# Kernel optimization log

Measured on AMD Instinct MI355X. Metric: run time of the kernel, lower is better.

The kernel has to match this reference:

```python
import jax, jax.numpy as jnp
import numpy as np

N = 8192
FEAT = 200
SEG = FEAT // 4  # 50
OUT = 300


def setup_inputs() -> dict:
    key = jax.random.key(0)
    ks = jax.random.split(key, 10)
    x = jax.random.normal(ks[0], (N, FEAT), dtype=jnp.float32)
    # row-normalized-ish dense adjacencies so activations stay O(1)
    A_S = jax.random.uniform(ks[1], (N, N), dtype=jnp.float32) / N
    A_F = jax.random.uniform(ks[2], (N, N), dtype=jnp.float32) / N
    gcn_W = jax.random.normal(ks[3], (SEG, SEG), dtype=jnp.float32) / np.sqrt(SEG)
    gcn_b = jnp.zeros((SEG,), dtype=jnp.float32)
    # 12 forget gates: order s1,s2,s3,f1,f2,f3,s1b,s2b,s3b,f1b,f2b,f3b
    gates_W = jax.random.normal(ks[4], (12, 2 * SEG, SEG), dtype=jnp.float32)
    gates_b = jax.random.normal(ks[5], (12, SEG), dtype=jnp.float32)
    proj_W = jax.random.normal(ks[6], (8 * SEG, OUT), dtype=jnp.float32) / np.sqrt(8 * SEG)
    proj_b = jnp.zeros((OUT,), dtype=jnp.float32)
    return {"x": x, "A_S": A_S, "A_F": A_F, "gcn_W": gcn_W, "gcn_b": gcn_b,
            "gates_W": gates_W, "gates_b": gates_b, "proj_W": proj_W, "proj_b": proj_b}


def _lgfm(x, A_S, A_F, gcn_W, gcn_b, gates_W, gates_b, proj_W, proj_b):
    seg = x.shape[1] // 4

    def gcn(h, A):
        # Kipf GraphConvolution: relu(A @ (h @ W) + b); dropout inactive (eval)
        return jax.nn.relu(A @ (h @ gcn_W) + gcn_b)

    def gate(i, h1, h2):
        a = jax.nn.sigmoid(jnp.concatenate([h1, h2], axis=1) @ gates_W[i] + gates_b[i])
        return a * h1

    GS1, GS2, GS3, GF1, GF2, GF3 = 0, 1, 2, 3, 4, 5
    GS1B, GS2B, GS3B, GF1B, GF2B, GF3B = 6, 7, 8, 9, 10, 11

    x1, x2, x3, x4 = x[:, :seg], x[:, seg:2 * seg], x[:, 2 * seg:3 * seg], x[:, 3 * seg:]

    # forward branch (F path then S gating)
    t1_XF1 = x1 + gcn(x1, A_F)
    t1_XS1 = gcn(x1, A_S)
    t1_XF2 = 0.2 * t1_XS1 + 0.8 * gcn(t1_XF1, A_F)
    t2_XF1 = x2 + gcn(x2, A_F)
    t2_XS1 = gcn(x2, A_S)
    t2_XS1 = t2_XS1 + gate(GS1, t1_XS1, t2_XS1)
    t2_XF2 = 0.2 * t2_XS1 + 0.8 * gcn(t2_XF1, A_F)
    t2_XF2 = gate(GF1, t1_XF2, t2_XF2) + t2_XF2
    t3_XF1 = 0.2 * x3 + 0.8 * gcn(x3, A_F)
    t3_XS1 = gcn(x3, A_S)
    t3_XS1 = t3_XS1 + gate(GS2, t2_XS1, t3_XS1)
    t3_XF2 = 0.2 * t3_XS1 + 0.8 * gcn(t3_XF1, A_F)
    t3_XF2 = gate(GF2, t2_XF2, t3_XF2) + t3_XF2
    t4_XF1 = x4 + gcn(x4, A_F)
    t4_XS1 = gcn(x4, A_S)
    t4_XS1 = t4_XS1 + gate(GS3, t3_XS1, t4_XS1)
    t4_XF2 = 0.2 * t4_XS1 + 0.8 * gcn(t4_XF1, A_F)
    t4_XF2 = gate(GF3, t3_XF2, t4_XF2) + t4_XF2

    # mirrored branch (S path then F gating)
    t1_XS1b = x1 + gcn(x1, A_S)
    t1_XF1b = gcn(x1, A_F)
    t1_XS2 = 0.2 * t1_XF1b + 0.8 * gcn(t1_XS1b, A_S)
    t2_XS1b = x2 + gcn(x2, A_S)
    t2_XF1b = gcn(x2, A_F)
    t2_XF1b = t2_XF1b + gate(GF1B, t1_XF1b, t2_XF1b)
    t2_XS2 = 0.2 * t2_XF1b + 0.8 * gcn(t2_XS1b, A_S)
    t2_XS2 = gate(GS1B, t1_XS2, t2_XS2) + t2_XS2
    t3_XS1b = 0.2 * x3 + 0.8 * gcn(x3, A_S)
    t3_XF1b = gcn(x3, A_F)
    t3_XF1b = t3_XF1b + gate(GF2B, t2_XF1b, t3_XF1b)
    t3_XS2 = 0.2 * t3_XF1b + 0.8 * gcn(t3_XS1b, A_S)
    t3_XS2 = gate(GS2B, t2_XS2, t3_XS2) + t3_XS2
    t4_XS1b = x4 + gcn(x4, A_S)
    t4_XF1b = gcn(x4, A_F)
    t4_XF1b = t4_XF1b + gate(GF3B, t3_XF1b, t4_XF1b)
    t4_XS2 = 0.2 * t4_XF1b + 0.8 * gcn(t4_XS1b, A_S)
    t4_XS2 = gate(GS3B, t3_XS2, t4_XS2) + t4_XS2

    h_L = jnp.concatenate([t1_XF2, t1_XS2, t2_XF2, t2_XS2,
                           t3_XF2, t3_XS2, t4_XF2, t4_XS2], axis=1)
    return h_L @ proj_W + proj_b


def reference(x, A_S, A_F, gcn_W, gcn_b, gates_W, gates_b, proj_W, proj_b):
    return _lgfm(x, A_S, A_F, gcn_W, gcn_b, gates_W, gates_b, proj_W, proj_b)
```

## Files before the change

### kernel.cpp

```cpp
#include <hip/hip_runtime.h>
#include <math.h>

typedef float float4v __attribute__((ext_vector_type(4)));
typedef __attribute__((ext_vector_type(4))) float f32x4;
typedef __attribute__((ext_vector_type(8))) short short8v;
typedef __attribute__((ext_vector_type(8))) unsigned short ushort8v;

#define NROW 8192
#define FEAT 200
#define OUTC 300
#define ZLD  256
#define HLK  448
#define HLN  384

__device__ __forceinline__ unsigned short f2bf(float x) {
  unsigned u = __float_as_uint(x);
  return (unsigned short)((u + 0x7fffu + ((u >> 16) & 1u)) >> 16);
}

__global__ __launch_bounds__(256) void conv2_bf16_kernel(
    const float* __restrict__ AF, const float* __restrict__ AS,
    unsigned short* __restrict__ AbF, unsigned short* __restrict__ AbS) {
  int blk = blockIdx.x;
  const float* A = (blk < 8192) ? AF : AS;
  unsigned short* Ab = (blk < 8192) ? AbF : AbS;
  size_t tid = (size_t)(blk & 8191) * 256 + threadIdx.x;
  const float4v* A4 = (const float4v*)A;
  ushort8v* O8 = (ushort8v*)Ab;
  for (size_t b = tid * 2; b < 16777216ull; b += (size_t)8192 * 256 * 2) {
    float4v v0 = __builtin_nontemporal_load(&A4[b]);
    float4v v1 = __builtin_nontemporal_load(&A4[b + 1]);
    ushort8v o;
    o[0] = f2bf(v0[0]); o[1] = f2bf(v0[1]); o[2] = f2bf(v0[2]); o[3] = f2bf(v0[3]);
    o[4] = f2bf(v1[0]); o[5] = f2bf(v1[1]); o[6] = f2bf(v1[2]); o[7] = f2bf(v1[3]);
    __builtin_nontemporal_store(o, &O8[b >> 1]);
  }
}

__global__ __launch_bounds__(256) void zmul_t_kernel(
    const float* __restrict__ x, const float* __restrict__ W,
    unsigned short* __restrict__ Zt) {
  __shared__ float Ws[2500];
  __shared__ float hs[16][200];
  __shared__ float zbuf[16][256];
  int t = threadIdx.x;
  int r0 = blockIdx.x * 16;
  for (int i = t; i < 2500; i += 256) Ws[i] = W[i];
  for (int i = t; i < 16 * FEAT; i += 256)
    hs[0][i] = x[(size_t)r0 * FEAT + i];
  __syncthreads();
  for (int i = t; i < 16 * 256; i += 256) {
    int row = i >> 8, j = i & 255;
    float acc = 0.f;
    if (j < FEAT) {
      int s = j / 50, jj = j % 50;
      const float* hrow = &hs[row][s * 50];
      #pragma unroll 5
      for (int k = 0; k < 50; ++k) acc += hrow[k] * Ws[k * 50 + jj];
    }
    zbuf[row][j] = acc;
  }
  __syncthreads();
  unsigned int* Ztu = (unsigned int*)Zt;
  for (int i = t; i < 256 * 8; i += 256) {
    int j = i >> 3, w2 = i & 7;
    unsigned int lo = f2bf(zbuf[2 * w2][j]);
    unsigned int hi = f2bf(zbuf[2 * w2 + 1][j]);
    Ztu[((j * NROW + r0) >> 1) + w2] = lo | (hi << 16);
  }
}

__global__ __launch_bounds__(256, 2) void gemm_pair_kernel(
    const unsigned short* __restrict__ AbF,
    const unsigned short* __restrict__ AbS,
    const unsigned short* __restrict__ ZtF,
    const unsigned short* __restrict__ ZtS,
    float* __restrict__ Cpart) {
  int d = blockIdx.x;
  int L = (d & 7) * 64 + (d >> 3);
  int mat = L & 1;
  int ks  = (L >> 1) & 1;
  int cb  = (L >> 2) & 1;
  int rb  = L >> 3;

  const unsigned short* __restrict__ Ab = mat ? AbS : AbF;
  const unsigned short* __restrict__ Zt = mat ? ZtS : ZtF;

  int t = threadIdx.x;
  int lane = t & 63, wv = t >> 6;
  int row0 = rb * 128, n0 = cb * 128, k0 = ks * 4096;

  __shared__ short As[2][128 * 64];
  __shared__ short Bs[2][128 * 64];

  int srcA[4], srcB[4], ldsDst[4];
  #pragma unroll
  for (int i = 0; i < 4; ++i) {
    int c = i * 256 + t;
    int m = c >> 3, sl = c & 7;
    int sw = ((sl ^ (m & 7)) * 8);
    srcA[i] = (row0 + m) * NROW + sw;
    srcB[i] = (n0 + m) * NROW + sw;
    ldsDst[i] = (i * 256 + wv * 64) * 8;
  }

#define STAGE_TILE(buf, kt)                                                          \
  {                                                                                  \
    _Pragma("unroll")                                                                \
    for (int i = 0; i < 4; ++i) {                                                    \
      __builtin_amdgcn_global_load_lds(                                              \
          (const __attribute__((address_space(1))) void*)(Ab + srcA[i] + (kt)),      \
          (__attribute__((address_space(3))) void*)(&As[buf][ldsDst[i]]), 16, 0, 0); \
      __builtin_amdgcn_global_load_lds(                                              \
          (const __attribute__((address_space(1))) void*)(Zt + srcB[i] + (kt)),      \
          (__attribute__((address_space(3))) void*)(&Bs[buf][ldsDst[i]]), 16, 0, 0); \
    }                                                                                \
  }

  f32x4 acc[4][4];
  #pragma unroll
  for (int i = 0; i < 4; ++i)
    #pragma unroll
    for (int j = 0; j < 4; ++j) acc[i][j] = (f32x4)0.f;

  int m0 = (wv >> 1) * 64, n0w = (wv & 1) * 64;
  int l15 = lane & 15, l4 = lane >> 4;

  int cur = 0;
  STAGE_TILE(0, k0)
  __syncthreads();

  for (int it = 0; it < 64; ++it) {
    if (it + 1 < 64) STAGE_TILE(cur ^ 1, k0 + (it + 1) * 64)

    #pragma unroll
    for (int kk = 0; kk < 2; ++kk) {
      int slot = kk * 4 + l4;
      short8v a[4], b[4];
      #pragma unroll
      for (int i = 0; i < 4; ++i) {
        int m = m0 + i * 16 + l15;
        a[i] = *(const short8v*)&As[cur][m * 64 + ((slot ^ (m & 7)) * 8)];
        int n = n0w + i * 16 + l15;
        b[i] = *(const short8v*)&Bs[cur][n * 64 + ((slot ^ (n & 7)) * 8)];
      }
      #pragma unroll
      for (int i = 0; i < 4; ++i)
        #pragma unroll
        for (int j = 0; j < 4; ++j)
          acc[i][j] = __builtin_amdgcn_mfma_f32_16x16x32_bf16(a[i], b[j], acc[i][j], 0, 0, 0);
    }
    __syncthreads();
    cur ^= 1;
  }
#undef STAGE_TILE

  int s = mat * 2 + ks;
  #pragma unroll
  for (int i = 0; i < 4; ++i) {
    #pragma unroll
    for (int j = 0; j < 4; ++j) {
      int c = n0 + n0w + j * 16 + l15;
      #pragma unroll
      for (int q = 0; q < 4; ++q) {
        int r = row0 + m0 + i * 16 + l4 * 4 + q;
        Cpart[((size_t)(s * NROW + r) << 8) + c] = acc[i][j][q];
      }
    }
  }
}

__global__ __launch_bounds__(256) void reduce_zmul_kernel(
    const float* __restrict__ Cpart, const float* __restrict__ bias,
    const float* __restrict__ x, const float* __restrict__ W,
    float* __restrict__ GF0, float* __restrict__ GS0,
    unsigned short* __restrict__ ZtF, unsigned short* __restrict__ ZtS) {
  __shared__ float Ws[2500];
  __shared__ float hs[16][200];
  __shared__ float zbuf[16][256];
  int t = threadIdx.x;
  int r0 = blockIdx.x * 16;
  int w = t >> 6, j = t & 63;
  bool act = j < 50;
  int rbase = r0 + w * 4;
  for (int i = t; i < 2500; i += 256) Ws[i] = W[i];

  const float alpha[4] = {1.f, 1.f, 0.2f, 1.f};
  const float beta[4]  = {1.f, 1.f, 0.8f, 1.f};
  float gf[4][4], gs[4][4];
  if (act) {
    float bv = bias[j];
    #pragma unroll
    for (int r = 0; r < 4; ++r)
      #pragma unroll
      for (int s = 0; s < 4; ++s) {
        int c = s * 50 + j;
        size_t base = (((size_t)(rbase + r)) << 8) + c;
        float vF = Cpart[base] + Cpart[base + (size_t)NROW * 256];
        float vS = Cpart[base + (size_t)2 * NROW * 256] + Cpart[base + (size_t)3 * NROW * 256];
        gf[r][s] = fmaxf(vF + bv, 0.f);
        gs[r][s] = fmaxf(vS + bv, 0.f);
        GF0[(size_t)(rbase + r) * FEAT + c] = gf[r][s];
        GS0[(size_t)(rbase + r) * FEAT + c] = gs[r][s];
      }
    #pragma unroll
    for (int r = 0; r < 4; ++r)
      #pragma unroll
      for (int s = 0; s < 4; ++s)
        hs[w * 4 + r][s * 50 + j] =
            alpha[s] * x[(size_t)(rbase + r) * FEAT + s * 50 + j] + beta[s] * gf[r][s];
  }
  __syncthreads();
  for (int i = t; i < 16 * 256; i += 256) {
    int row = i >> 8, jj = i & 255;
    float acc = 0.f;
    if (jj < FEAT) {
      int s = jj / 50, j2 = jj % 50;
      const float* hrow = &hs[row][s * 50];
      #pragma unroll 5
      for (int k = 0; k < 50; ++k) acc += hrow[k] * Ws[k * 50 + j2];
    }
    zbuf[row][jj] = acc;
  }
  __syncthreads();
  {
    unsigned int* Ztu = (unsigned int*)ZtF;
    for (int i = t; i < 256 * 8; i += 256) {
      int j2 = i >> 3, w2 = i & 7;
      unsigned int lo = f2bf(zbuf[2 * w2][j2]);
      unsigned int hi = f2bf(zbuf[2 * w2 + 1][j2]);
      Ztu[((j2 * NROW + r0) >> 1) + w2] = lo | (hi << 16);
    }
  }
  if (act) {
    #pragma unroll
    for (int r = 0; r < 4; ++r)
      #pragma unroll
      for (int s = 0; s < 4; ++s)
        hs[w * 4 + r][s * 50 + j] =
            alpha[s] * x[(size_t)(rbase + r) * FEAT + s * 50 + j] + beta[s] * gs[r][s];
  }
  __syncthreads();
  for (int i = t; i < 16 * 256; i += 256) {
    int row = i >> 8, jj = i & 255;
    float acc = 0.f;
    if (jj < FEAT) {
      int s = jj / 50, j2 = jj % 50;
      const float* hrow = &hs[row][s * 50];
      #pragma unroll 5
      for (int k = 0; k < 50; ++k) acc += hrow[k] * Ws[k * 50 + j2];
    }
    zbuf[row][jj] = acc;
  }
  __syncthreads();
  {
    unsigned int* Ztu = (unsigned int*)ZtS;
    for (int i = t; i < 256 * 8; i += 256) {
      int j2 = i >> 3, w2 = i & 7;
      unsigned int lo = f2bf(zbuf[2 * w2][j2]);
      unsigned int hi = f2bf(zbuf[2 * w2 + 1][j2]);
      Ztu[((j2 * NROW + r0) >> 1) + w2] = lo | (hi << 16);
    }
  }
}

__device__ __forceinline__ void gate4(const float* __restrict__ gWi, const float* __restrict__ gbi,
                                      float* hsw, float* Wg, int t, int j, bool act,
                                      const float* h1, const float* h2, float* aout) {
  if (act) {
    #pragma unroll
    for (int r = 0; r < 4; ++r) { hsw[r * 128 + j] = h1[r]; hsw[r * 128 + 64 + j] = h2[r]; }
  }
  {
    const float4v* src = (const float4v*)gWi;
    float4v* dst = (float4v*)Wg;
    #pragma unroll
    for (int u = 0; u < 5; ++u) {
      int i = t + 256 * u;
      if (i < 1250) dst[i] = src[i];
    }
  }
  __syncthreads();
  float acc0 = 0.f, acc1 = 0.f, acc2 = 0.f, acc3 = 0.f;
  if (act) {
    float bv = gbi[j];
    acc0 = bv; acc1 = bv; acc2 = bv; acc3 = bv;
    #pragma unroll 2
    for (int k = 0; k < 50; ++k) {
      float wv = Wg[k * 50 + j];
      acc0 += hsw[0 * 128 + k] * wv;
      acc1 += hsw[1 * 128 + k] * wv;
      acc2 += hsw[2 * 128 + k] * wv;
      acc3 += hsw[3 * 128 + k] * wv;
    }
    #pragma unroll 2
    for (int k = 0; k < 50; ++k) {
      float wv = Wg[(50 + k) * 50 + j];
      acc0 += hsw[0 * 128 + 64 + k] * wv;
      acc1 += hsw[1 * 128 + 64 + k] * wv;
      acc2 += hsw[2 * 128 + 64 + k] * wv;
      acc3 += hsw[3 * 128 + 64 + k] * wv;
    }
  }
  __syncthreads();
  float accs[4] = {acc0, acc1, acc2, acc3};
  #pragma unroll
  for (int r = 0; r < 4; ++r) {
    float a = 1.f / (1.f + expf(-accs[r]));
    aout[r] = a * h1[r];
  }
}

__global__ __launch_bounds__(256) void reduce_chain_kernel(
    const float* __restrict__ Cpart, const float* __restrict__ bias,
    const float* __restrict__ GF0, const float* __restrict__ GS0,
    const float* __restrict__ gW, const float* __restrict__ gb,
    unsigned short* __restrict__ hLb) {
  __shared__ float hsb[4 * 512];
  __shared__ float Wg[5000];
  int t = threadIdx.x;
  int w = t >> 6, j = t & 63;
  bool act = j < 50;
  float* hsw = &hsb[w * 512];
  int rbase = blockIdx.x * 16 + w * 4;

  float gf0[4][4], gs0[4][4], gf1[4][4], gs1[4][4];
  if (act) {
    float bv = bias[j];
    #pragma unroll
    for (int r = 0; r < 4; ++r)
      #pragma unroll
      for (int s = 0; s < 4; ++s) {
        int c = s * 50 + j;
        size_t base = (((size_t)(rbase + r)) << 8) + c;
        float vF = Cpart[base] + Cpart[base + (size_t)NROW * 256];
        float vS = Cpart[base + (size_t)2 * NROW * 256] + Cpart[base + (size_t)3 * NROW * 256];
        gf1[r][s] = fmaxf(vF + bv, 0.f);
        gs1[r][s] = fmaxf(vS + bv, 0.f);
        gf0[r][s] = GF0[(size_t)(rbase + r) * FEAT + c];
        gs0[r][s] = GS0[(size_t)(rbase + r) * FEAT + c];
      }
  }
  if (!act) {
    for (int p = j - 50; p < 48; p += 14)
      #pragma unroll
      for (int r = 0; r < 4; ++r)
        hLb[(size_t)(rbase + r) * HLK + 400 + p] = 0;
  }

  float xf2[4], xs1[4], pre[4], a[4], h1t[4], h2t[4];
  #pragma unroll
  for (int r = 0; r < 4; ++r) xf2[r] = 0.2f * gs0[r][0] + 0.8f * gf1[r][0];
  if (act) {
    #pragma unroll
    for (int r = 0; r < 4; ++r) hLb[(size_t)(rbase + r) * HLK + 0 + j] = f2bf(xf2[r]);
  }
  #pragma unroll
  for (int r = 0; r < 4; ++r) { h1t[r] = gs0[r][0]; h2t[r] = gs0[r][1]; }
  gate4(gW + 0 * 5000, gb + 0 * 50, hsw, Wg, t, j, act, h1t, h2t, a);
  #pragma unroll
  for (int r = 0; r < 4; ++r) xs1[r] = gs0[r][1] + a[r];
  #pragma unroll
  for (int r = 0; r < 4; ++r) pre[r] = 0.2f * xs1[r] + 0.8f * gf1[r][1];
  gate4(gW + 3 * 5000, gb + 3 * 50, hsw, Wg, t, j, act, xf2, pre, a);
  #pragma unroll
  for (int r = 0; r < 4; ++r) xf2[r] = a[r] + pre[r];
  if (act) {
    #pragma unroll
    for (int r = 0; r < 4; ++r) hLb[(size_t)(rbase + r) * HLK + 100 + j] = f2bf(xf2[r]);
  }
  #pragma unroll
  for (int r = 0; r < 4; ++r) { h1t[r] = xs1[r]; h2t[r] = gs0[r][2]; }
  gate4(gW + 1 * 5000, gb + 1 * 50, hsw, Wg, t, j, act, h1t, h2t, a);
  #pragma unroll
  for (int r = 0; r < 4; ++r) xs1[r] = gs0[r][2] + a[r];
  #pragma unroll
  for (int r = 0; r < 4; ++r) pre[r] = 0.2f * xs1[r] + 0.8f * gf1[r][2];
  gate4(gW + 4 * 5000, gb + 4 * 50, hsw, Wg, t, j, act, xf2, pre, a);
  #pragma unroll
  for (int r = 0; r < 4; ++r) xf2[r] = a[r] + pre[r];
  if (act) {
    #pragma unroll
    for (int r = 0; r < 4; ++r) hLb[(size_t)(rbase + r) * HLK + 200 + j] = f2bf(xf2[r]);
  }
  #pragma unroll
  for (int r = 0; r < 4; ++r) { h1t[r] = xs1[r]; h2t[r] = gs0[r][3]; }
  gate4(gW + 2 * 5000, gb + 2 * 50, hsw, Wg, t, j, act, h1t, h2t, a);
  #pragma unroll
  for (int r = 0; r < 4; ++r) xs1[r] = gs0[r][3] + a[r];
  #pragma unroll
  for (int r = 0; r < 4; ++r) pre[r] = 0.2f * xs1[r] + 0.8f * gf1[r][3];
  gate4(gW + 5 * 5000, gb + 5 * 50, hsw, Wg, t, j, act, xf2, pre, a);
  #pragma unroll
  for (int r = 0; r < 4; ++r) xf2[r] = a[r] + pre[r];
  if (act) {
    #pragma unroll
    for (int r = 0; r < 4; ++r) hLb[(size_t)(rbase + r) * HLK + 300 + j] = f2bf(xf2[r]);
  }

  float xs2[4], xf1b[4];
  #pragma unroll
  for (int r = 0; r < 4; ++r) xs2[r] = 0.2f * gf0[r][0] + 0.8f * gs1[r][0];
  if (act) {
    #pragma unroll
    for (int r = 0; r < 4; ++r) hLb[(size_t)(rbase + r) * HLK + 50 + j] = f2bf(xs2[r]);
  }
  #pragma unroll
  for (int r = 0; r < 4; ++r) { h1t[r] = gf0[r][0]; h2t[r] = gf0[r][1]; }
  gate4(gW + 9 * 5000, gb + 9 * 50, hsw, Wg, t, j, act, h1t, h2t, a);
  #pragma unroll
  for (int r = 0; r < 4; ++r) xf1b[r] = gf0[r][1] + a[r];
  #pragma unroll
  for (int r = 0; r < 4; ++r) pre[r] = 0.2f * xf1b[r] + 0.8f * gs1[r][1];
  gate4(gW + 6 * 5000, gb + 6 * 50, hsw, Wg, t, j, act, xs2, pre, a);
  #pragma unroll
  for (int r = 0; r < 4; ++r) xs2[r] = a[r] + pre[r];
  if (act) {
    #pragma unroll
    for (int r = 0; r < 4; ++r) hLb[(size_t)(rbase + r) * HLK + 150 + j] = f2bf(xs2[r]);
  }
  #pragma unroll
  for (int r = 0; r < 4; ++r) { h1t[r] = xf1b[r]; h2t[r] = gf0[r][2]; }
  gate4(gW + 10 * 5000, gb + 10 * 50, hsw, Wg, t, j, act, h1t, h2t, a);
  #pragma unroll
  for (int r = 0; r < 4; ++r) xf1b[r] = gf0[r][2] + a[r];
  #pragma unroll
  for (int r = 0; r < 4; ++r) pre[r] = 0.2f * xf1b[r] + 0.8f * gs1[r][2];
  gate4(gW + 7 * 5000, gb + 7 * 50, hsw, Wg, t, j, act, xs2, pre, a);
  #pragma unroll
  for (int r = 0; r < 4; ++r) xs2[r] = a[r] + pre[r];
  if (act) {
    #pragma unroll
    for (int r = 0; r < 4; ++r) hLb[(size_t)(rbase + r) * HLK + 250 + j] = f2bf(xs2[r]);
  }
  #pragma unroll
  for (int r = 0; r < 4; ++r) { h1t[r] = xf1b[r]; h2t[r] = gf0[r][3]; }
  gate4(gW + 11 * 5000, gb + 11 * 50, hsw, Wg, t, j, act, h1t, h2t, a);
  #pragma unroll
  for (int r = 0; r < 4; ++r) xf1b[r] = gf0[r][3] + a[r];
  #pragma unroll
  for (int r = 0; r < 4; ++r) pre[r] = 0.2f * xf1b[r] + 0.8f * gs1[r][3];
  gate4(gW + 8 * 5000, gb + 8 * 50, hsw, Wg, t, j, act, xs2, pre, a);
  #pragma unroll
  for (int r = 0; r < 4; ++r) xs2[r] = a[r] + pre[r];
  if (act) {
    #pragma unroll
    for (int r = 0; r < 4; ++r) hLb[(size_t)(rbase + r) * HLK + 350 + j] = f2bf(xs2[r]);
  }
}

__global__ __launch_bounds__(256) void wconv_kernel(
    const float* __restrict__ pW, unsigned short* __restrict__ Wtb) {
  int i = blockIdx.x * 256 + threadIdx.x;
  if (i >= HLN * HLK) return;
  int n = i / HLK, k = i % HLK;
  float v = (n < OUTC && k < 400) ? pW[k * OUTC + n] : 0.f;
  Wtb[i] = f2bf(v);
}

__global__ __launch_bounds__(256, 2) void proj_gemm_kernel(
    const unsigned short* __restrict__ hLb,
    const unsigned short* __restrict__ Wtb,
    const float* __restrict__ pb, float* __restrict__ outp) {
  int d = blockIdx.x;
  int L = (d & 7) * 24 + (d >> 3);
  int rb = L / 3, cb = L % 3;

  int t = threadIdx.x;
  int lane = t & 63, wv = t >> 6;
  int row0 = rb * 128, n0 = cb * 128;

  __shared__ short As[2][128 * 64];
  __shared__ short Bs[2][128 * 64];

  int srcA[4], srcB[4], ldsDst[4];
  #pragma unroll
  for (int i = 0; i < 4; ++i) {
    int c = i * 256 + t;
    int m = c >> 3, sl = c & 7;
    int sw = ((sl ^ (m & 7)) * 8);
    srcA[i] = (row0 + m) * HLK + sw;
    srcB[i] = (n0 + m) * HLK + sw;
    ldsDst[i] = (i * 256 + wv * 64) * 8;
  }

#define STAGE_TILE(buf, kt)                                                          \
  {                                                                                  \
    _Pragma("unroll")                                                                \
    for (int i = 0; i < 4; ++i) {                                                    \
      __builtin_amdgcn_global_load_lds(                                              \
          (const __attribute__((address_space(1))) void*)(hLb + srcA[i] + (kt)),     \
          (__attribute__((address_space(3))) void*)(&As[buf][ldsDst[i]]), 16, 0, 0); \
      __builtin_amdgcn_global_load_lds(                                              \
          (const __attribute__((address_space(1))) void*)(Wtb + srcB[i] + (kt)),     \
          (__attribute__((address_space(3))) void*)(&Bs[buf][ldsDst[i]]), 16, 0, 0); \
    }                                                                                \
  }

  f32x4 acc[4][4];
  #pragma unroll
  for (int i = 0; i < 4; ++i)
    #pragma unroll
    for (int j = 0; j < 4; ++j) acc[i][j] = (f32x4)0.f;

  int m0 = (wv >> 1) * 64, n0w = (wv & 1) * 64;
  int l15 = lane & 15, l4 = lane >> 4;

  int cur = 0;
  STAGE_TILE(0, 0)
  __syncthreads();

  for (int it = 0; it < 7; ++it) {
    if (it + 1 < 7) STAGE_TILE(cur ^ 1, (it + 1) * 64)

    #pragma unroll
    for (int kk = 0; kk < 2; ++kk) {
      int slot = kk * 4 + l4;
      short8v a[4], b[4];
      #pragma unroll
      for (int i = 0; i < 4; ++i) {
        int m = m0 + i * 16 + l15;
        a[i] = *(const short8v*)&As[cur][m * 64 + ((slot ^ (m & 7)) * 8)];
        int n = n0w + i * 16 + l15;
        b[i] = *(const short8v*)&Bs[cur][n * 64 + ((slot ^ (n & 7)) * 8)];
      }
      #pragma unroll
      for (int i = 0; i < 4; ++i)
        #pragma unroll
        for (int j = 0; j < 4; ++j)
          acc[i][j] = __builtin_amdgcn_mfma_f32_16x16x32_bf16(a[i], b[j], acc[i][j], 0, 0, 0);
    }
    __syncthreads();
    cur ^= 1;
  }
#undef STAGE_TILE

  #pragma unroll
  for (int i = 0; i < 4; ++i) {
    #pragma unroll
    for (int j = 0; j < 4; ++j) {
      int c = n0 + n0w + j * 16 + l15;
      if (c < OUTC) {
        float b = pb[c];
        #pragma unroll
        for (int q = 0; q < 4; ++q) {
          int r = row0 + m0 + i * 16 + l4 * 4 + q;
          outp[(size_t)r * OUTC + c] = acc[i][j][q] + b;
        }
      }
    }
  }
}

__global__ __launch_bounds__(256) void zmul_f32_kernel(
    const float* __restrict__ x, const float* __restrict__ g,
    const float* __restrict__ W,
    float a0, float a1, float a2, float a3,
    float b0, float b1, float b2, float b3,
    float* __restrict__ Zp) {
  __shared__ float Ws[2500];
  __shared__ float hs[200];
  int t = threadIdx.x;
  for (int i = t; i < 2500; i += 256) Ws[i] = W[i];
  float alpha[4] = {a0, a1, a2, a3};
  float beta[4]  = {b0, b1, b2, b3};
  int s  = (t < 200) ? (t / 50) : 0;
  int jj = (t < 200) ? (t % 50) : 0;
  int r0 = blockIdx.x * 32;
  for (int rr = 0; rr < 32; ++rr) {
    int row = r0 + rr;
    __syncthreads();
    if (t < 200) hs[t] = alpha[s] * x[row * FEAT + t] + beta[s] * g[row * FEAT + t];
    __syncthreads();
    float acc = 0.f;
    if (t < 200) {
      const float* hrow = &hs[s * 50];
      #pragma unroll 5
      for (int k = 0; k < 50; ++k) acc += hrow[k] * Ws[k * 50 + jj];
    }
    Zp[row * ZLD + t] = (t < 200) ? acc : 0.f;
  }
}

#define BM 64
#define BN 64
#define BK 32
#define ALD 68
__global__ __launch_bounds__(256) void gemm_relu_kernel(
    const float* __restrict__ A, const float* __restrict__ Zp,
    const float* __restrict__ bias, float* __restrict__ C) {
  int wg  = blockIdx.x;
  int swz = (wg & 7) * 64 + (wg >> 3);
  int rb  = swz >> 2;
  int cb  = swz & 3;
  int t   = threadIdx.x;
  int rt  = t >> 4, ct = t & 15;
  __shared__ __align__(16) float As[BK][ALD];
  __shared__ __align__(16) float Zs[BK][BN];
  float acc[4][4];
  #pragma unroll
  for (int i = 0; i < 4; ++i)
    #pragma unroll
    for (int j = 0; j < 4; ++j) acc[i][j] = 0.f;
  const int row0 = rb * BM, col0 = cb * BN;
  int ar = t >> 3;
  int ak = (t & 7) * 4;
  int zr = t >> 4;
  int zc = (t & 15) * 4;
  const float4v* A4 = (const float4v*)A;
  const float4v* Z4 = (const float4v*)Zp;
  float4v a0, a1, z0, z1;
  a0 = A4[((size_t)(row0 + ar) * NROW + 0 + ak) >> 2];
  a1 = A4[((size_t)(row0 + ar + 32) * NROW + 0 + ak) >> 2];
  z0 = Z4[((0 + zr) * ZLD + col0 + zc) >> 2];
  z1 = Z4[((0 + zr + 16) * ZLD + col0 + zc) >> 2];
  for (int kt = 0; kt < NROW; kt += BK) {
    __syncthreads();
    #pragma unroll
    for (int u = 0; u < 4; ++u) As[ak + u][ar] = a0[u];
    #pragma unroll
    for (int u = 0; u < 4; ++u) As[ak + u][ar + 32] = a1[u];
    *(float4v*)&Zs[zr][zc]      = z0;
    *(float4v*)&Zs[zr + 16][zc] = z1;
    __syncthreads();
    int kn = kt + BK;
    if (kn < NROW) {
      a0 = A4[((size_t)(row0 + ar) * NROW + kn + ak) >> 2];
      a1 = A4[((size_t)(row0 + ar + 32) * NROW + kn + ak) >> 2];
      z0 = Z4[((kn + zr) * ZLD + col0 + zc) >> 2];
      z1 = Z4[((kn + zr + 16) * ZLD + col0 + zc) >> 2];
    }
    #pragma unroll
    for (int k = 0; k < BK; ++k) {
      float4v av = *(const float4v*)&As[k][rt * 4];
      float4v zv = *(const float4v*)&Zs[k][ct * 4];
      #pragma unroll
      for (int i = 0; i < 4; ++i)
        #pragma unroll
        for (int j = 0; j < 4; ++j) acc[i][j] += av[i] * zv[j];
    }
  }
  #pragma unroll
  for (int i = 0; i < 4; ++i) {
    int grow = row0 + rt * 4 + i;
    #pragma unroll
    for (int j = 0; j < 4; ++j) {
      int gcol = col0 + ct * 4 + j;
      if (gcol < FEAT) {
        float v = acc[i][j] + bias[gcol % 50];
        C[(size_t)grow * FEAT + gcol] = fmaxf(v, 0.f);
      }
    }
  }
}

__global__ __launch_bounds__(256) void chain_top_kernel(
    const float* __restrict__ GS0, const float* __restrict__ GF1,
    const float* __restrict__ gW, const float* __restrict__ gb,
    unsigned short* __restrict__ hLb) {
  __shared__ float hsb[4 * 512];
  __shared__ float Wg[5000];
  int t = threadIdx.x;
  int w = t >> 6, j = t & 63;
  bool act = j < 50;
  float* hsw = &hsb[w * 512];
  int rbase = blockIdx.x * 16 + w * 4;
  float gs[4][4], gf[4][4];
  #pragma unroll
  for (int r = 0; r < 4; ++r)
    #pragma unroll
    for (int s = 0; s < 4; ++s) { gs[r][s] = 0.f; gf[r][s] = 0.f; }
  if (act) {
    #pragma unroll
    for (int r = 0; r < 4; ++r)
      #pragma unroll
      for (int s = 0; s < 4; ++s) {
        gs[r][s] = GS0[(size_t)(rbase + r) * FEAT + s * 50 + j];
        gf[r][s] = GF1[(size_t)(rbase + r) * FEAT + s * 50 + j];
      }
  }
  float xf2[4], xs1[4], pre[4], a[4], h1t[4], h2t[4];
  #pragma unroll
  for (int r = 0; r < 4; ++r) xf2[r] = 0.2f * gs[r][0] + 0.8f * gf[r][0];
  if (act) {
    #pragma unroll
    for (int r = 0; r < 4; ++r) hLb[(size_t)(rbase + r) * HLK + 0 + j] = f2bf(xf2[r]);
  }
  #pragma unroll
  for (int r = 0; r < 4; ++r) { h1t[r] = gs[r][0]; h2t[r] = gs[r][1]; }
  gate4(gW + 0 * 5000, gb + 0 * 50, hsw, Wg, t, j, act, h1t, h2t, a);
  #pragma unroll
  for (int r = 0; r < 4; ++r) xs1[r] = gs[r][1] + a[r];
  #pragma unroll
  for (int r = 0; r < 4; ++r) pre[r] = 0.2f * xs1[r] + 0.8f * gf[r][1];
  gate4(gW + 3 * 5000, gb + 3 * 50, hsw, Wg, t, j, act, xf2, pre, a);
  #pragma unroll
  for (int r = 0; r < 4; ++r) xf2[r] = a[r] + pre[r];
  if (act) {
    #pragma unroll
    for (int r = 0; r < 4; ++r) hLb[(size_t)(rbase + r) * HLK + 100 + j] = f2bf(xf2[r]);
  }
  #pragma unroll
  for (int r = 0; r < 4; ++r) { h1t[r] = xs1[r]; h2t[r] = gs[r][2]; }
  gate4(gW + 1 * 5000, gb + 1 * 50, hsw, Wg, t, j, act, h1t, h2t, a);
  #pragma unroll
  for (int r = 0; r < 4; ++r) xs1[r] = gs[r][2] + a[r];
  #pragma unroll
  for (int r = 0; r < 4; ++r) pre[r] = 0.2f * xs1[r] + 0.8f * gf[r][2];
  gate4(gW + 4 * 5000, gb + 4 * 50, hsw, Wg, t, j, act, xf2, pre, a);
  #pragma unroll
  for (int r = 0; r < 4; ++r) xf2[r] = a[r] + pre[r];
  if (act) {
    #pragma unroll
    for (int r = 0; r < 4; ++r) hLb[(size_t)(rbase + r) * HLK + 200 + j] = f2bf(xf2[r]);
  }
  #pragma unroll
  for (int r = 0; r < 4; ++r) { h1t[r] = xs1[r]; h2t[r] = gs[r][3]; }
  gate4(gW + 2 * 5000, gb + 2 * 50, hsw, Wg, t, j, act, h1t, h2t, a);
  #pragma unroll
  for (int r = 0; r < 4; ++r) xs1[r] = gs[r][3] + a[r];
  #pragma unroll
  for (int r = 0; r < 4; ++r) pre[r] = 0.2f * xs1[r] + 0.8f * gf[r][3];
  gate4(gW + 5 * 5000, gb + 5 * 50, hsw, Wg, t, j, act, xf2, pre, a);
  #pragma unroll
  for (int r = 0; r < 4; ++r) xf2[r] = a[r] + pre[r];
  if (act) {
    #pragma unroll
    for (int r = 0; r < 4; ++r) hLb[(size_t)(rbase + r) * HLK + 300 + j] = f2bf(xf2[r]);
  }
}

__global__ __launch_bounds__(256) void chain_bottom_kernel(
    const float* __restrict__ GF0, const float* __restrict__ GS1,
    const float* __restrict__ gW, const float* __restrict__ gb,
    unsigned short* __restrict__ hLb) {
  __shared__ float hsb[4 * 512];
  __shared__ float Wg[5000];
  int t = threadIdx.x;
  int w = t >> 6, j = t & 63;
  bool act = j < 50;
  float* hsw = &hsb[w * 512];
  int rbase = blockIdx.x * 16 + w * 4;
  float gf0[4][4], gs1[4][4];
  #pragma unroll
  for (int r = 0; r < 4; ++r)
    #pragma unroll
    for (int s = 0; s < 4; ++s) { gf0[r][s] = 0.f; gs1[r][s] = 0.f; }
  if (act) {
    #pragma unroll
    for (int r = 0; r < 4; ++r)
      #pragma unroll
      for (int s = 0; s < 4; ++s) {
        gf0[r][s] = GF0[(size_t)(rbase + r) * FEAT + s * 50 + j];
        gs1[r][s] = GS1[(size_t)(rbase + r) * FEAT + s * 50 + j];
      }
  }
  float xs2[4], xf1b[4], pre[4], a[4], h1t[4], h2t[4];
  #pragma unroll
  for (int r = 0; r < 4; ++r) xs2[r] = 0.2f * gf0[r][0] + 0.8f * gs1[r][0];
  if (act) {
    #pragma unroll
    for (int r = 0; r < 4; ++r) hLb[(size_t)(rbase + r) * HLK + 50 + j] = f2bf(xs2[r]);
  }
  #pragma unroll
  for (int r = 0; r < 4; ++r) { h1t[r] = gf0[r][0]; h2t[r] = gf0[r][1]; }
  gate4(gW + 9 * 5000, gb + 9 * 50, hsw, Wg, t, j, act, h1t, h2t, a);
  #pragma unroll
  for (int r = 0; r < 4; ++r) xf1b[r] = gf0[r][1] + a[r];
  #pragma unroll
  for (int r = 0; r < 4; ++r) pre[r] = 0.2f * xf1b[r] + 0.8f * gs1[r][1];
  gate4(gW + 6 * 5000, gb + 6 * 50, hsw, Wg, t, j, act, xs2, pre, a);
  #pragma unroll
  for (int r = 0; r < 4; ++r) xs2[r] = a[r] + pre[r];
  if (act) {
    #pragma unroll
    for (int r = 0; r < 4; ++r) hLb[(size_t)(rbase + r) * HLK + 150 + j] = f2bf(xs2[r]);
  }
  #pragma unroll
  for (int r = 0; r < 4; ++r) { h1t[r] = xf1b[r]; h2t[r] = gf0[r][2]; }
  gate4(gW + 10 * 5000, gb + 10 * 50, hsw, Wg, t, j, act, h1t, h2t, a);
  #pragma unroll
  for (int r = 0; r < 4; ++r) xf1b[r] = gf0[r][2] + a[r];
  #pragma unroll
  for (int r = 0; r < 4; ++r) pre[r] = 0.2f * xf1b[r] + 0.8f * gs1[r][2];
  gate4(gW + 7 * 5000, gb + 7 * 50, hsw, Wg, t, j, act, xs2, pre, a);
  #pragma unroll
  for (int r = 0; r < 4; ++r) xs2[r] = a[r] + pre[r];
  if (act) {
    #pragma unroll
    for (int r = 0; r < 4; ++r) hLb[(size_t)(rbase + r) * HLK + 250 + j] = f2bf(xs2[r]);
  }
  #pragma unroll
  for (int r = 0; r < 4; ++r) { h1t[r] = xf1b[r]; h2t[r] = gf0[r][3]; }
  gate4(gW + 11 * 5000, gb + 11 * 50, hsw, Wg, t, j, act, h1t, h2t, a);
  #pragma unroll
  for (int r = 0; r < 4; ++r) xf1b[r] = gf0[r][3] + a[r];
  #pragma unroll
  for (int r = 0; r < 4; ++r) pre[r] = 0.2f * xf1b[r] + 0.8f * gs1[r][3];
  gate4(gW + 8 * 5000, gb + 8 * 50, hsw, Wg, t, j, act, xs2, pre, a);
  #pragma unroll
  for (int r = 0; r < 4; ++r) xs2[r] = a[r] + pre[r];
  if (act) {
    #pragma unroll
    for (int r = 0; r < 4; ++r) hLb[(size_t)(rbase + r) * HLK + 350 + j] = f2bf(xs2[r]);
  }
}

extern "C" void kernel_launch(void* const* d_in, const int* in_sizes, int n_in,
                              void* d_out, int out_size, void* d_ws, size_t ws_size,
                              hipStream_t stream) {
  const float* x       = (const float*)d_in[0];
  const float* A_S     = (const float*)d_in[1];
  const float* A_F     = (const float*)d_in[2];
  const float* gcn_W   = (const float*)d_in[3];
  const float* gcn_b   = (const float*)d_in[4];
  const float* gates_W = (const float*)d_in[5];
  const float* gates_b = (const float*)d_in[6];
  const float* proj_W  = (const float*)d_in[7];
  const float* proj_b  = (const float*)d_in[8];
  float* out = (float*)d_out;

  const size_t szAb    = (size_t)NROW * NROW * 2;
  const size_t szZt    = (size_t)256 * NROW * 2;
  const size_t szCpart = (size_t)4 * NROW * 256 * 4;
  const size_t szG     = (size_t)NROW * FEAT * 4;
  const size_t szHLb   = (size_t)NROW * HLK * 2;
  const size_t szWtb   = (size_t)HLN * HLK * 2;
  const size_t need = 2 * szAb + 3 * szZt + szCpart + 2 * szG + szHLb + szWtb;

  if (ws_size >= need) {
    char* w = (char*)d_ws;
    unsigned short* AbF  = (unsigned short*)w;           w += szAb;
    unsigned short* AbS  = (unsigned short*)w;           w += szAb;
    unsigned short* Zt0  = (unsigned short*)w;           w += szZt;
    unsigned short* Zt1F = (unsigned short*)w;           w += szZt;
    unsigned short* Zt1S = (unsigned short*)w;           w += szZt;
    float* Cpart = (float*)w;                            w += szCpart;
    float* GF0 = (float*)w;                              w += szG;
    float* GS0 = (float*)w;                              w += szG;
    unsigned short* hLb = (unsigned short*)w;            w += szHLb;
    unsigned short* Wtb = (unsigned short*)w;

    conv2_bf16_kernel<<<16384, 256, 0, stream>>>(A_F, A_S, AbF, AbS);
    wconv_kernel<<<(HLN * HLK + 255) / 256, 256, 0, stream>>>(proj_W, Wtb);
    zmul_t_kernel<<<512, 256, 0, stream>>>(x, gcn_W, Zt0);

    gemm_pair_kernel<<<512, 256, 0, stream>>>(AbF, AbS, Zt0, Zt0, Cpart);
    reduce_zmul_kernel<<<512, 256, 0, stream>>>(Cpart, gcn_b, x, gcn_W, GF0, GS0, Zt1F, Zt1S);

    gemm_pair_kernel<<<512, 256, 0, stream>>>(AbF, AbS, Zt1F, Zt1S, Cpart);
    reduce_chain_kernel<<<512, 256, 0, stream>>>(Cpart, gcn_b, GF0, GS0, gates_W, gates_b, hLb);

    proj_gemm_kernel<<<192, 256, 0, stream>>>(hLb, Wtb, proj_b, out);
  } else {
    char* w = (char*)d_ws;
    float* Z   = (float*)w;                              w += (size_t)NROW * ZLD * 4;
    float* GF0 = (float*)w;                              w += szG;
    float* GS0 = (float*)w;                              w += szG;
    float* GF1 = (float*)w;                              w += szG;
    float* GS1 = (float*)w;                              w += szG;
    unsigned short* hLb = (unsigned short*)w;            w += szHLb;
    unsigned short* Wtb = (unsigned short*)w;

    hipMemsetAsync(hLb, 0, szHLb, stream);
    wconv_kernel<<<(HLN * HLK + 255) / 256, 256, 0, stream>>>(proj_W, Wtb);

    zmul_f32_kernel<<<256, 256, 0, stream>>>(x, x, gcn_W, 1.f, 1.f, 1.f, 1.f, 0.f, 0.f, 0.f, 0.f, Z);
    gemm_relu_kernel<<<512, 256, 0, stream>>>(A_F, Z, gcn_b, GF0);
    gemm_relu_kernel<<<512, 256, 0, stream>>>(A_S, Z, gcn_b, GS0);
    zmul_f32_kernel<<<256, 256, 0, stream>>>(x, GF0, gcn_W, 1.f, 1.f, 0.2f, 1.f, 1.f, 1.f, 0.8f, 1.f, Z);
    gemm_relu_kernel<<<512, 256, 0, stream>>>(A_F, Z, gcn_b, GF1);
    zmul_f32_kernel<<<256, 256, 0, stream>>>(x, GS0, gcn_W, 1.f, 1.f, 0.2f, 1.f, 1.f, 1.f, 0.8f, 1.f, Z);
    gemm_relu_kernel<<<512, 256, 0, stream>>>(A_S, Z, gcn_b, GS1);

    chain_top_kernel<<<512, 256, 0, stream>>>(GS0, GF1, gates_W, gates_b, hLb);
    chain_bottom_kernel<<<512, 256, 0, stream>>>(GF0, GS1, gates_W, gates_b, hLb);
    proj_gemm_kernel<<<192, 256, 0, stream>>>(hLb, Wtb, proj_b, out);
  }
}
```

Measured before the change: 520.2 us.

## Fuse fp32-to-bf16 adjacency conversion into the pair GEMM's A-tile staging

Removes the separate pass that converted both dense adjacency matrices to bf16. The GEMM now loads fp32 A tiles into registers, converts them with packed bf16 conversion instructions, and writes them swizzled into LDS. The B operand keeps the async load-to-LDS path. This removes one full write and reread of the bf16 copies and frees workspace. In exchange, each GEMM reads twice as many bytes for A, the loads go through registers, and register pressure rises.

```diff
diff --git a/kernel.cpp b/kernel.cpp
--- a/kernel.cpp
+++ b/kernel.cpp
@@ -16,25 +16,6 @@
 __device__ __forceinline__ unsigned short f2bf(float x) {
   unsigned u = __float_as_uint(x);
   return (unsigned short)((u + 0x7fffu + ((u >> 16) & 1u)) >> 16);
-}
-
-__global__ __launch_bounds__(256) void conv2_bf16_kernel(
-    const float* __restrict__ AF, const float* __restrict__ AS,
-    unsigned short* __restrict__ AbF, unsigned short* __restrict__ AbS) {
-  int blk = blockIdx.x;
-  const float* A = (blk < 8192) ? AF : AS;
-  unsigned short* Ab = (blk < 8192) ? AbF : AbS;
-  size_t tid = (size_t)(blk & 8191) * 256 + threadIdx.x;
-  const float4v* A4 = (const float4v*)A;
-  ushort8v* O8 = (ushort8v*)Ab;
-  for (size_t b = tid * 2; b < 16777216ull; b += (size_t)8192 * 256 * 2) {
-    float4v v0 = __builtin_nontemporal_load(&A4[b]);
-    float4v v1 = __builtin_nontemporal_load(&A4[b + 1]);
-    ushort8v o;
-    o[0] = f2bf(v0[0]); o[1] = f2bf(v0[1]); o[2] = f2bf(v0[2]); o[3] = f2bf(v0[3]);
-    o[4] = f2bf(v1[0]); o[5] = f2bf(v1[1]); o[6] = f2bf(v1[2]); o[7] = f2bf(v1[3]);
-    __builtin_nontemporal_store(o, &O8[b >> 1]);
-  }
 }
 
 __global__ __launch_bounds__(256) void zmul_t_kernel(
@@ -70,9 +51,8 @@
   }
 }
 
-__global__ __launch_bounds__(256, 2) void gemm_pair_kernel(
-    const unsigned short* __restrict__ AbF,
-    const unsigned short* __restrict__ AbS,
+__global__ __launch_bounds__(256, 2) void gemm_cvt_pair_kernel(
+    const float* __restrict__ AF, const float* __restrict__ AS,
     const unsigned short* __restrict__ ZtF,
     const unsigned short* __restrict__ ZtS,
     float* __restrict__ Cpart) {
@@ -83,7 +63,7 @@
   int cb  = (L >> 2) & 1;
   int rb  = L >> 3;
 
-  const unsigned short* __restrict__ Ab = mat ? AbS : AbF;
+  const float* __restrict__ A = mat ? AS : AF;
   const unsigned short* __restrict__ Zt = mat ? ZtS : ZtF;
 
   int t = threadIdx.x;
@@ -93,28 +73,54 @@
   __shared__ short As[2][128 * 64];
   __shared__ short Bs[2][128 * 64];
 
-  int srcA[4], srcB[4], ldsDst[4];
+  int srcAf[4], dstA[4];
+  #pragma unroll
+  for (int i = 0; i < 4; ++i) {
+    int cc = i * 256 + t;
+    int m = cc >> 3, s = cc & 7;
+    srcAf[i] = (row0 + m) * NROW + s * 8;
+    dstA[i] = m * 64 + ((s ^ (m & 7)) * 8);
+  }
+  int srcB[4], ldsDstB[4];
   #pragma unroll
   for (int i = 0; i < 4; ++i) {
     int c = i * 256 + t;
     int m = c >> 3, sl = c & 7;
-    int sw = ((sl ^ (m & 7)) * 8);
-    srcA[i] = (row0 + m) * NROW + sw;
-    srcB[i] = (n0 + m) * NROW + sw;
-    ldsDst[i] = (i * 256 + wv * 64) * 8;
-  }
-
-#define STAGE_TILE(buf, kt)                                                          \
-  {                                                                                  \
-    _Pragma("unroll")                                                                \
-    for (int i = 0; i < 4; ++i) {                                                    \
-      __builtin_amdgcn_global_load_lds(                                              \
-          (const __attribute__((address_space(1))) void*)(Ab + srcA[i] + (kt)),      \
-          (__attribute__((address_space(3))) void*)(&As[buf][ldsDst[i]]), 16, 0, 0); \
-      __builtin_amdgcn_global_load_lds(                                              \
-          (const __attribute__((address_space(1))) void*)(Zt + srcB[i] + (kt)),      \
-          (__attribute__((address_space(3))) void*)(&Bs[buf][ldsDst[i]]), 16, 0, 0); \
-    }                                                                                \
+    srcB[i] = (n0 + m) * NROW + ((sl ^ (m & 7)) * 8);
+    ldsDstB[i] = (i * 256 + wv * 64) * 8;
+  }
+
+  f32x4 ar0[4], ar1[4];
+
+#define STAGE_B(buf, kt)                                                              \
+  {                                                                                   \
+    _Pragma("unroll")                                                                 \
+    for (int i = 0; i < 4; ++i)                                                       \
+      __builtin_amdgcn_global_load_lds(                                               \
+          (const __attribute__((address_space(1))) void*)(Zt + srcB[i] + (kt)),       \
+          (__attribute__((address_space(3))) void*)(&Bs[buf][ldsDstB[i]]), 16, 0, 0); \
+  }
+#define LOAD_A(kt)                                         \
+  {                                                        \
+    _Pragma("unroll")                                      \
+    for (int i = 0; i < 4; ++i) {                          \
+      ar0[i] = *(const f32x4*)&A[srcAf[i] + (kt)];         \
+      ar1[i] = *(const f32x4*)&A[srcAf[i] + (kt) + 4];     \
+    }                                                      \
+  }
+#define WRITE_A(buf)                                                                    \
+  {                                                                                     \
+    _Pragma("unroll")                                                                   \
+    for (int i = 0; i < 4; ++i) {                                                       \
+      unsigned u0_, u1_, u2_, u3_;                                                      \
+      asm("v_cvt_pk_bf16_f32 %0, %1, %2" : "=v"(u0_) : "v"(ar0[i][0]), "v"(ar0[i][1]));\
+      asm("v_cvt_pk_bf16_f32 %0, %1, %2" : "=v"(u1_) : "v"(ar0[i][2]), "v"(ar0[i][3]));\
+      asm("v_cvt_pk_bf16_f32 %0, %1, %2" : "=v"(u2_) : "v"(ar1[i][0]), "v"(ar1[i][1]));\
+      asm("v_cvt_pk_bf16_f32 %0, %1, %2" : "=v"(u3_) : "v"(ar1[i][2]), "v"(ar1[i][3]));\
+      union { unsigned u[4]; short8v v; } pk_;                                          \
+      pk_.u[0] = u0_; pk_.u[1] = u1_; pk_.u[2] = u2_; pk_.u[3] = u3_;                   \
+      *(short8v*)&As[buf][dstA[i]] = pk_.v;                                             \
+    }                                                                                   \
   }
 
   f32x4 acc[4][4];
@@ -127,11 +133,16 @@
   int l15 = lane & 15, l4 = lane >> 4;
 
   int cur = 0;
-  STAGE_TILE(0, k0)
+  LOAD_A(k0)
+  STAGE_B(0, k0)
+  WRITE_A(0)
   __syncthreads();
 
   for (int it = 0; it < 64; ++it) {
-    if (it + 1 < 64) STAGE_TILE(cur ^ 1, k0 + (it + 1) * 64)
+    if (it + 1 < 64) {
+      STAGE_B(cur ^ 1, k0 + (it + 1) * 64)
+      LOAD_A(k0 + (it + 1) * 64)
+    }
 
     #pragma unroll
     for (int kk = 0; kk < 2; ++kk) {
@@ -150,10 +161,14 @@
         for (int j = 0; j < 4; ++j)
           acc[i][j] = __builtin_amdgcn_mfma_f32_16x16x32_bf16(a[i], b[j], acc[i][j], 0, 0, 0);
     }
+
+    if (it + 1 < 64) WRITE_A(cur ^ 1)
     __syncthreads();
     cur ^= 1;
   }
-#undef STAGE_TILE
+#undef STAGE_B
+#undef LOAD_A
+#undef WRITE_A
 
   int s = mat * 2 + ks;
   #pragma unroll
@@ -820,18 +835,15 @@
   const float* proj_b  = (const float*)d_in[8];
   float* out = (float*)d_out;
 
-  const size_t szAb    = (size_t)NROW * NROW * 2;
   const size_t szZt    = (size_t)256 * NROW * 2;
   const size_t szCpart = (size_t)4 * NROW * 256 * 4;
   const size_t szG     = (size_t)NROW * FEAT * 4;
   const size_t szHLb   = (size_t)NROW * HLK * 2;
   const size_t szWtb   = (size_t)HLN * HLK * 2;
-  const size_t need = 2 * szAb + 3 * szZt + szCpart + 2 * szG + szHLb + szWtb;
+  const size_t need = 3 * szZt + szCpart + 2 * szG + szHLb + szWtb;
 
   if (ws_size >= need) {
     char* w = (char*)d_ws;
-    unsigned short* AbF  = (unsigned short*)w;           w += szAb;
-    unsigned short* AbS  = (unsigned short*)w;           w += szAb;
     unsigned short* Zt0  = (unsigned short*)w;           w += szZt;
     unsigned short* Zt1F = (unsigned short*)w;           w += szZt;
     unsigned short* Zt1S = (unsigned short*)w;           w += szZt;
@@ -841,14 +853,13 @@
     unsigned short* hLb = (unsigned short*)w;            w += szHLb;
     unsigned short* Wtb = (unsigned short*)w;
 
-    conv2_bf16_kernel<<<16384, 256, 0, stream>>>(A_F, A_S, AbF, AbS);
     wconv_kernel<<<(HLN * HLK + 255) / 256, 256, 0, stream>>>(proj_W, Wtb);
     zmul_t_kernel<<<512, 256, 0, stream>>>(x, gcn_W, Zt0);
 
-    gemm_pair_kernel<<<512, 256, 0, stream>>>(AbF, AbS, Zt0, Zt0, Cpart);
+    gemm_cvt_pair_kernel<<<512, 256, 0, stream>>>(A_F, A_S, Zt0, Zt0, Cpart);
     reduce_zmul_kernel<<<512, 256, 0, stream>>>(Cpart, gcn_b, x, gcn_W, GF0, GS0, Zt1F, Zt1S);
 
-    gemm_pair_kernel<<<512, 256, 0, stream>>>(AbF, AbS, Zt1F, Zt1S, Cpart);
+    gemm_cvt_pair_kernel<<<512, 256, 0, stream>>>(A_F, A_S, Zt1F, Zt1S, Cpart);
     reduce_chain_kernel<<<512, 256, 0, stream>>>(Cpart, gcn_b, GF0, GS0, gates_W, gates_b, hLb);
 
     proj_gemm_kernel<<<192, 256, 0, stream>>>(hLb, Wtb, proj_b, out);
```

After: 486.1 us. 6.6% less time.
